# Performance work log

Hardware: AMD Instinct MI355X
Metric: run time of the kernel (lower is better)

## Reference

```python
import jax, jax.numpy as jnp
import numpy as np
from itertools import product

G = 96          # voxel grid side
B = 2           # batch samples
N_PER = 60000   # occupied voxels per sample
N = B * N_PER
C_IN = 64
C_OUT = 1
NUM_BLOCKS = 2
EPS = 1e-5


def _build_kernel_map():
    """Emulate MinkowskiEngine's coordinate hash map for a k=3, stride=1, 3D conv.
    Returns batch_ids [N], and per-offset (in_idx, out_idx) padded to N with sentinel N."""
    rng = np.random.default_rng(0)
    side = G - 2  # coords in [1, G-2] so offset coords never wrap
    keys_list = []
    for b in range(B):
        lin = rng.choice(side ** 3, size=N_PER, replace=False)
        x = lin // (side * side) + 1
        y = (lin // side) % side + 1
        z = lin % side + 1
        keys_list.append(b * G ** 3 + x * G * G + y * G + z)
    keys = np.concatenate(keys_list)
    batch_ids = np.repeat(np.arange(B), N_PER).astype(np.int32)
    order = np.argsort(keys)
    skeys = keys[order]
    in_idx = np.full((27, N), N, np.int32)   # sentinel N -> zero-padded feature row
    out_idx = np.full((27, N), N, np.int32)  # sentinel N -> dropped output row
    for k, (dx, dy, dz) in enumerate(product((-1, 0, 1), repeat=3)):
        nk = keys + dx * G * G + dy * G + dz  # neighbor coordinate key per output voxel
        pos = np.searchsorted(skeys, nk)
        pc = np.clip(pos, 0, N - 1)
        valid = skeys[pc] == nk
        m = int(valid.sum())
        in_idx[k, :m] = order[pc[valid]]
        out_idx[k, :m] = np.nonzero(valid)[0]
    return batch_ids, in_idx, out_idx


def instance_norm(f, batch_ids, num_batches):
    # per-sample, per-channel normalization over all voxels of each sample (ME InstanceNorm, no affine)
    cnt = jax.ops.segment_sum(jnp.ones((f.shape[0],), f.dtype), batch_ids, num_segments=num_batches)
    mean = jax.ops.segment_sum(f, batch_ids, num_segments=num_batches) / cnt[:, None]
    fc = f - mean[batch_ids]
    var = jax.ops.segment_sum(fc * fc, batch_ids, num_segments=num_batches) / cnt[:, None]
    return fc * jax.lax.rsqrt(var + EPS)[batch_ids]


def sparse_conv(f, w, in_idx, out_idx, bias=None):
    # gather-matmul-scatter per kernel offset; w: [27, Cin, Cout]
    n = f.shape[0]
    fpad = jnp.concatenate([f, jnp.zeros((1, f.shape[1]), f.dtype)], axis=0)
    out = jnp.zeros((n + 1, w.shape[-1]), f.dtype)
    for k in range(w.shape[0]):  # static 27-iteration loop over kernel offsets
        out = out.at[out_idx[k]].add(fpad[in_idx[k]] @ w[k])
    out = out[:n]
    if bias is not None:
        out = out + bias
    return out


def setup_inputs() -> dict:
    batch_ids, in_idx, out_idx = _build_kernel_map()
    key = jax.random.key(0)
    k0, k1, k2, k3 = jax.random.split(key, 4)
    feats = jax.random.normal(k0, (N, C_IN), dtype=jnp.float32)
    w_blocks = jax.random.normal(k1, (NUM_BLOCKS, 2, 27, C_IN, C_IN), dtype=jnp.float32) * 0.02
    w_final = jax.random.normal(k2, (27, C_IN, C_OUT), dtype=jnp.float32) * 0.02
    b_final = jax.random.normal(k3, (C_OUT,), dtype=jnp.float32) * 0.02
    return {
        "feats": feats,
        "w_blocks": w_blocks,
        "w_final": w_final,
        "b_final": b_final,
        "in_idx": jnp.asarray(in_idx),
        "out_idx": jnp.asarray(out_idx),
        "batch_ids": jnp.asarray(batch_ids),
        "batch_size": B,
    }


def reference(feats, w_blocks, w_final, b_final, in_idx, out_idx, batch_ids, batch_size):
    # InstanceNorm + ReLU
    x = jax.nn.relu(instance_norm(feats, batch_ids, batch_size))
    # SparseBasicBlocks: conv -> IN -> relu -> conv -> IN -> +res -> relu
    for b in range(w_blocks.shape[0]):
        res = x
        h = sparse_conv(x, w_blocks[b, 0], in_idx, out_idx)
        h = jax.nn.relu(instance_norm(h, batch_ids, batch_size))
        h = sparse_conv(h, w_blocks[b, 1], in_idx, out_idx)
        h = instance_norm(h, batch_ids, batch_size)
        x = jax.nn.relu(h + res)
    # final conv with bias
    return sparse_conv(x, w_final, in_idx, out_idx, bias=b_final)
```

## Files before the change

kernel.cpp:

```cpp
#include <hip/hip_runtime.h>

#define NPTS 120000
#define NROW 120064
#define NB   60000
#define TAPS 27
#define NBLK (NROW / 128)

typedef short  short8 __attribute__((ext_vector_type(8)));
typedef float  f32x4  __attribute__((ext_vector_type(4)));
typedef unsigned int u32;

__device__ __forceinline__ float bf2f(unsigned short u) {
  unsigned v = ((unsigned)u) << 16;
  float f; __builtin_memcpy(&f, &v, 4); return f;
}
__device__ __forceinline__ unsigned short f2bf(float f) {
  unsigned v; __builtin_memcpy(&v, &f, 4);
  v = v + 0x7FFFu + ((v >> 16) & 1u);
  return (unsigned short)(v >> 16);
}

__device__ __forceinline__ int xcd_swz(int orig, int nwg) {
  int q = nwg >> 3, r = nwg & 7;
  int x = orig & 7, i = orig >> 3;
  return (x < r ? x * (q + 1) : r * (q + 1) + (x - r) * q) + i;
}

__global__ __launch_bounds__(256) void k_init(int* __restrict__ nbr,
                                              const float* __restrict__ w,
                                              unsigned short* __restrict__ wp,
                                              float* __restrict__ SMa) {
  int b = blockIdx.x, t = threadIdx.x;
  if (b < 12663) {
    nbr[b * 256 + t] = -1;
    return;
  }
  b -= 12663;
  if (b < 1728) {
    int g = b * 256 + t;
    int e = g & 7, l = (g >> 3) & 63, f = (g >> 9) & 7, rest = g >> 12;
    int tt = f >> 1, h = f & 1;
    int kk = h * 32 + (l >> 4) * 8 + e;
    int cc = tt * 16 + (l & 15);
    wp[g] = f2bf(w[(rest * 64 + kk) * 64 + cc]);
    return;
  }
  if (t < 1280) SMa[t] = 0.f;
}

__global__ __launch_bounds__(256) void k_build_nbr(const int* __restrict__ oi,
                                                   const int* __restrict__ ii,
                                                   int* __restrict__ nbr) {
  int g = blockIdx.x * 256 + threadIdx.x;
  if (g >= TAPS * NPTS) return;
  int o = oi[g];
  if (o < NPTS) nbr[(g / NPTS) * NROW + o] = ii[g];
}

__global__ __launch_bounds__(256) void k_stats1_f32(const float* __restrict__ F,
                                                    float* __restrict__ SM) {
  int lane = threadIdx.x & 63, wave = threadIdx.x >> 6;
  int batch = blockIdx.x >> 7, bb = blockIdx.x & 127;
  const float* Fb = F + (size_t)batch * NB * 64;
  float s = 0.f, ss = 0.f;
  for (int r = bb * 4 + wave; r < NB; r += 512) {
    float v = Fb[(size_t)r * 64 + lane];
    s += v; ss += v * v;
  }
  __shared__ float ls[4][64], lss[4][64];
  ls[wave][lane] = s; lss[wave][lane] = ss;
  __syncthreads();
  if (threadIdx.x < 64) {
    float S  = ls[0][lane] + ls[1][lane] + ls[2][lane] + ls[3][lane];
    float SS = lss[0][lane] + lss[1][lane] + lss[2][lane] + lss[3][lane];
    atomicAdd(&SM[(batch * 2 + 0) * 64 + lane], S);
    atomicAdd(&SM[(batch * 2 + 1) * 64 + lane], SS);
  }
}

__global__ __launch_bounds__(256) void k_apply_f2b(const float* __restrict__ F,
                                                   const float* __restrict__ SM,
                                                   unsigned short* __restrict__ O) {
  int i = blockIdx.x * 256 + threadIdx.x;
  int r = i >> 3, cb = (i & 7) * 8;
  int b = (r >= NB) ? 1 : 0;
  f32x4 v0 = *((const f32x4*)F + i * 2);
  f32x4 v1 = *((const f32x4*)F + i * 2 + 1);
  short8 o;
#pragma unroll
  for (int e = 0; e < 8; ++e) {
    float mean = SM[(b * 2 + 0) * 64 + cb + e] * (1.f / NB);
    float var  = SM[(b * 2 + 1) * 64 + cb + e] * (1.f / NB) - mean * mean;
    float rstd = rsqrtf(var + 1e-5f);
    float x = (e < 4) ? v0[e & 3] : v1[e & 3];
    o[e] = (short)f2bf(fmaxf((x - mean) * rstd, 0.f));
  }
  *((short8*)O + i) = o;
}

__global__ __launch_bounds__(256) void k_apply_bf(const unsigned short* __restrict__ F,
                                                  const float* __restrict__ SM,
                                                  unsigned short* __restrict__ O) {
  int i = blockIdx.x * 256 + threadIdx.x;
  int r = i >> 3, cb = (i & 7) * 8;
  int b = (r >= NB) ? 1 : 0;
  short8 v = *((const short8*)F + i);
  short8 o;
#pragma unroll
  for (int e = 0; e < 8; ++e) {
    float mean = SM[(b * 2 + 0) * 64 + cb + e] * (1.f / NB);
    float var  = SM[(b * 2 + 1) * 64 + cb + e] * (1.f / NB) - mean * mean;
    float rstd = rsqrtf(var + 1e-5f);
    float f = (bf2f((unsigned short)v[e]) - mean) * rstd;
    o[e] = (short)f2bf(fmaxf(f, 0.f));
  }
  *((short8*)O + i) = o;
}

__global__ __launch_bounds__(256) void k_apply_res_bf(const unsigned short* __restrict__ H2,
                                                      const float* __restrict__ SM,
                                                      unsigned short* __restrict__ X) {
  int i = blockIdx.x * 256 + threadIdx.x;
  int r = i >> 3, cb = (i & 7) * 8;
  int b = (r >= NB) ? 1 : 0;
  short8 v = *((const short8*)H2 + i);
  short8 xv = *((const short8*)X + i);
  short8 o;
#pragma unroll
  for (int e = 0; e < 8; ++e) {
    float mean = SM[(b * 2 + 0) * 64 + cb + e] * (1.f / NB);
    float var  = SM[(b * 2 + 1) * 64 + cb + e] * (1.f / NB) - mean * mean;
    float rstd = rsqrtf(var + 1e-5f);
    float f = (bf2f((unsigned short)v[e]) - mean) * rstd + bf2f((unsigned short)xv[e]);
    o[e] = (short)f2bf(fmaxf(f, 0.f));
  }
  *((short8*)X + i) = o;
}

__global__ __launch_bounds__(256) void k_conv64s(const unsigned short* __restrict__ X,
                                                 const unsigned short* __restrict__ WP,
                                                 const int* __restrict__ nbr,
                                                 unsigned short* __restrict__ Y,
                                                 float* __restrict__ SM) {
  const int blk = xcd_swz(blockIdx.x, NBLK);
  const int lane = threadIdx.x & 63, wave = threadIdx.x >> 6;
  const int j0w = blk * 128 + wave * 32;
  const int lrow = lane & 15, lk = lane >> 4;
  f32x4 acc[2][4];
#pragma unroll
  for (int g = 0; g < 2; ++g)
#pragma unroll
    for (int c = 0; c < 4; ++c) acc[g][c] = (f32x4){0.f, 0.f, 0.f, 0.f};

  for (int k = 0; k < TAPS; ++k) {
    const int* np = nbr + (size_t)k * NROW + j0w + lrow;
    int i0 = np[0], i1 = np[16];
    if (__ballot(i0 >= 0 || i1 >= 0) == 0ull) continue;
    short8 a00 = {0,0,0,0,0,0,0,0}, a01 = {0,0,0,0,0,0,0,0};
    short8 a10 = {0,0,0,0,0,0,0,0}, a11 = {0,0,0,0,0,0,0,0};
    if (i0 >= 0) {
      const unsigned short* rp = X + (size_t)i0 * 64 + lk * 8;
      a00 = *(const short8*)rp; a01 = *(const short8*)(rp + 32);
    }
    if (i1 >= 0) {
      const unsigned short* rp = X + (size_t)i1 * 64 + lk * 8;
      a10 = *(const short8*)rp; a11 = *(const short8*)(rp + 32);
    }
    const unsigned short* wpk = WP + k * 4096 + lane * 8;
#pragma unroll
    for (int ct = 0; ct < 4; ++ct) {
      short8 b0 = *(const short8*)(wpk + ct * 1024);
      short8 b1 = *(const short8*)(wpk + ct * 1024 + 512);
      acc[0][ct] = __builtin_amdgcn_mfma_f32_16x16x32_bf16(a00, b0, acc[0][ct], 0, 0, 0);
      acc[0][ct] = __builtin_amdgcn_mfma_f32_16x16x32_bf16(a01, b1, acc[0][ct], 0, 0, 0);
      acc[1][ct] = __builtin_amdgcn_mfma_f32_16x16x32_bf16(a10, b0, acc[1][ct], 0, 0, 0);
      acc[1][ct] = __builtin_amdgcn_mfma_f32_16x16x32_bf16(a11, b1, acc[1][ct], 0, 0, 0);
    }
  }

#pragma unroll
  for (int g = 0; g < 2; ++g) {
    unsigned short* yp = Y + (size_t)(j0w + g * 16 + lk * 4) * 64 + lrow;
#pragma unroll
    for (int r = 0; r < 4; ++r) {
      yp[r * 64 +  0] = f2bf(acc[g][0][r]);
      yp[r * 64 + 16] = f2bf(acc[g][1][r]);
      yp[r * 64 + 32] = f2bf(acc[g][2][r]);
      yp[r * 64 + 48] = f2bf(acc[g][3][r]);
    }
  }

  float s[4][2], q[4][2];
#pragma unroll
  for (int ct = 0; ct < 4; ++ct) { s[ct][0] = s[ct][1] = q[ct][0] = q[ct][1] = 0.f; }
#pragma unroll
  for (int g = 0; g < 2; ++g) {
    int rowbase = j0w + g * 16 + lk * 4;
#pragma unroll
    for (int r = 0; r < 4; ++r) {
      int bt = (rowbase + r) >= NB;
#pragma unroll
      for (int ct = 0; ct < 4; ++ct) {
        float v = acc[g][ct][r];
        s[ct][bt] += v; q[ct][bt] += v * v;
      }
    }
  }
  __shared__ float sred[4][4][4][64];
#pragma unroll
  for (int ct = 0; ct < 4; ++ct)
#pragma unroll
    for (int b = 0; b < 2; ++b) {
      sred[wave][lk][b * 2 + 0][ct * 16 + lrow] = s[ct][b];
      sred[wave][lk][b * 2 + 1][ct * 16 + lrow] = q[ct][b];
    }
  __syncthreads();
  int t = threadIdx.x;
  float S = 0.f;
#pragma unroll
  for (int w = 0; w < 4; ++w)
#pragma unroll
    for (int l2 = 0; l2 < 4; ++l2)
      S += sred[w][l2][t >> 6][t & 63];
  atomicAdd(&SM[t], S);
}

__global__ __launch_bounds__(256) void k_dfin(const unsigned short* __restrict__ X,
                                              const float* __restrict__ WF,
                                              float* __restrict__ D) {
  const int lane = threadIdx.x & 63, wave = threadIdx.x >> 6;
  const int j0 = blockIdx.x * 64 + wave * 16;
  const int lrow = lane & 15, lk = lane >> 4;
  const unsigned short* rp = X + (size_t)(j0 + lrow) * 64 + lk * 8;
  short8 a0 = *(const short8*)rp;
  short8 a1 = *(const short8*)(rp + 32);
  short8 b[2][2];
#pragma unroll
  for (int ct = 0; ct < 2; ++ct) {
    int col = ct * 16 + lrow;
#pragma unroll
    for (int h = 0; h < 2; ++h) {
#pragma unroll
      for (int e = 0; e < 8; ++e)
        b[ct][h][e] = (col < TAPS) ? (short)f2bf(WF[col * 64 + h * 32 + lk * 8 + e]) : (short)0;
    }
  }
  f32x4 acc0 = {0,0,0,0}, acc1 = {0,0,0,0};
  acc0 = __builtin_amdgcn_mfma_f32_16x16x32_bf16(a0, b[0][0], acc0, 0, 0, 0);
  acc0 = __builtin_amdgcn_mfma_f32_16x16x32_bf16(a1, b[0][1], acc0, 0, 0, 0);
  acc1 = __builtin_amdgcn_mfma_f32_16x16x32_bf16(a0, b[1][0], acc1, 0, 0, 0);
  acc1 = __builtin_amdgcn_mfma_f32_16x16x32_bf16(a1, b[1][1], acc1, 0, 0, 0);
  float* dp0 = D + (size_t)lrow * NROW + j0 + lk * 4;
  float* dp1 = D + (size_t)(16 + lrow) * NROW + j0 + lk * 4;
#pragma unroll
  for (int r = 0; r < 4; ++r) { dp0[r] = acc0[r]; dp1[r] = acc1[r]; }
}

__global__ __launch_bounds__(256) void k_gfin(const float* __restrict__ D,
                                              const int* __restrict__ nbr,
                                              const float* __restrict__ BF,
                                              float* __restrict__ out) {
  int j = xcd_swz(blockIdx.x, NROW / 256) * 256 + threadIdx.x;
  if (j >= NPTS) return;
  float acc = BF[0];
#pragma unroll
  for (int k = 0; k < TAPS; ++k) {
    int idx = nbr[(size_t)k * NROW + j];
    if (idx >= 0) acc += D[(size_t)k * NROW + idx];
  }
  out[j] = acc;
}

extern "C" void kernel_launch(void* const* d_in, const int* in_sizes, int n_in,
                              void* d_out, int out_size, void* d_ws, size_t ws_size,
                              hipStream_t stream) {
  (void)in_sizes; (void)n_in; (void)out_size; (void)ws_size;
  const float* feats = (const float*)d_in[0];
  const float* wblk  = (const float*)d_in[1];
  const float* wfin  = (const float*)d_in[2];
  const float* bfin  = (const float*)d_in[3];
  const int* in_idx  = (const int*)d_in[4];
  const int* out_idx = (const int*)d_in[5];

  char* p = (char*)d_ws;
  size_t off = 0;
  auto carve = [&](size_t bytes) {
    void* r = p + off; off += (bytes + 255) & ~(size_t)255; return r;
  };
  int*            nbr = (int*)carve((size_t)TAPS * NROW * 4);
  unsigned short* Xb  = (unsigned short*)carve((size_t)NROW * 64 * 2);
  unsigned short* Hb  = (unsigned short*)carve((size_t)NROW * 64 * 2);
  unsigned short* H2b = (unsigned short*)carve((size_t)NROW * 64 * 2);
  unsigned short* WP  = (unsigned short*)carve(108u * 4096u * 2);
  float*          D   = (float*)carve((size_t)32 * NROW * 4);
  float*          SMa = (float*)carve(5 * 256 * 4);

  float* SM0 = SMa;
  float* SM1 = SMa + 256;
  float* SM2 = SMa + 512;
  float* SM3 = SMa + 768;
  float* SM4 = SMa + 1024;

  k_init<<<12663 + 1728 + 1, 256, 0, stream>>>(nbr, wblk, WP, SMa);
  k_build_nbr<<<(TAPS * NPTS + 255) / 256, 256, 0, stream>>>(out_idx, in_idx, nbr);

  k_stats1_f32<<<256, 256, 0, stream>>>(feats, SM0);
  k_apply_f2b<<<3750, 256, 0, stream>>>(feats, SM0, Xb);

  k_conv64s<<<NBLK, 256, 0, stream>>>(Xb, WP + 0 * 110592, nbr, Hb, SM1);
  k_apply_bf<<<3750, 256, 0, stream>>>(Hb, SM1, Hb);
  k_conv64s<<<NBLK, 256, 0, stream>>>(Hb, WP + 1 * 110592, nbr, H2b, SM2);
  k_apply_res_bf<<<3750, 256, 0, stream>>>(H2b, SM2, Xb);

  k_conv64s<<<NBLK, 256, 0, stream>>>(Xb, WP + 2 * 110592, nbr, Hb, SM3);
  k_apply_bf<<<3750, 256, 0, stream>>>(Hb, SM3, Hb);
  k_conv64s<<<NBLK, 256, 0, stream>>>(Hb, WP + 3 * 110592, nbr, H2b, SM4);
  k_apply_res_bf<<<3750, 256, 0, stream>>>(H2b, SM4, Xb);

  k_dfin<<<NROW / 64, 256, 0, stream>>>(Xb, wfin, D);
  k_gfin<<<NROW / 256, 256, 0, stream>>>(D, nbr, bfin, (float*)d_out);
}
```

Baseline: 474.9 us.

## Fuse instance-norm+ReLU into next conv's gather, prefetch neighbor indices, drop XCD swizzle

Removes the standalone k_apply_bf pass by normalizing and ReLU-ing gathered bf16 rows inside the second conv of each block, using per-channel scale/shift precomputed from the first conv's statistics. The neighbor indices for the next tap are loaded one iteration ahead to hide their latency. The XCD block swizzle is removed from the conv and final-gather kernels. Each gathered row is now normalized up to 27 times instead of once, which adds ALU work in the conv inner loop. Dropping the swizzle may change L2 locality.

```diff
diff --git a/kernel.cpp b/kernel.cpp
--- a/kernel.cpp
+++ b/kernel.cpp
@@ -8,6 +8,7 @@
 
 typedef short  short8 __attribute__((ext_vector_type(8)));
 typedef float  f32x4  __attribute__((ext_vector_type(4)));
+typedef int    int4v  __attribute__((ext_vector_type(4)));
 typedef unsigned int u32;
 
 __device__ __forceinline__ float bf2f(unsigned short u) {
@@ -20,10 +21,19 @@
   return (unsigned short)(v >> 16);
 }
 
-__device__ __forceinline__ int xcd_swz(int orig, int nwg) {
-  int q = nwg >> 3, r = nwg & 7;
-  int x = orig & 7, i = orig >> 3;
-  return (x < r ? x * (q + 1) : r * (q + 1) + (x - r) * q) + i;
+__device__ __forceinline__ short8 norm8(short8 v, const float* A, const float* B) {
+  float f[8];
+#pragma unroll
+  for (int e = 0; e < 8; ++e)
+    f[e] = fmaxf(fmaf(bf2f((unsigned short)v[e]), A[e], B[e]), 0.f);
+  int4v p;
+#pragma unroll
+  for (int j = 0; j < 4; ++j) {
+    u32 r;
+    asm("v_cvt_pk_bf16_f32 %0, %1, %2" : "=v"(r) : "v"(f[2 * j]), "v"(f[2 * j + 1]));
+    p[j] = (int)r;
+  }
+  union { int4v i; short8 s; } u; u.i = p; return u.s;
 }
 
 __global__ __launch_bounds__(256) void k_init(int* __restrict__ nbr,
@@ -98,25 +108,6 @@
   *((short8*)O + i) = o;
 }
 
-__global__ __launch_bounds__(256) void k_apply_bf(const unsigned short* __restrict__ F,
-                                                  const float* __restrict__ SM,
-                                                  unsigned short* __restrict__ O) {
-  int i = blockIdx.x * 256 + threadIdx.x;
-  int r = i >> 3, cb = (i & 7) * 8;
-  int b = (r >= NB) ? 1 : 0;
-  short8 v = *((const short8*)F + i);
-  short8 o;
-#pragma unroll
-  for (int e = 0; e < 8; ++e) {
-    float mean = SM[(b * 2 + 0) * 64 + cb + e] * (1.f / NB);
-    float var  = SM[(b * 2 + 1) * 64 + cb + e] * (1.f / NB) - mean * mean;
-    float rstd = rsqrtf(var + 1e-5f);
-    float f = (bf2f((unsigned short)v[e]) - mean) * rstd;
-    o[e] = (short)f2bf(fmaxf(f, 0.f));
-  }
-  *((short8*)O + i) = o;
-}
-
 __global__ __launch_bounds__(256) void k_apply_res_bf(const unsigned short* __restrict__ H2,
                                                       const float* __restrict__ SM,
                                                       unsigned short* __restrict__ X) {
@@ -137,45 +128,73 @@
   *((short8*)X + i) = o;
 }
 
-__global__ __launch_bounds__(256) void k_conv64s(const unsigned short* __restrict__ X,
+template <int NORM>
+__global__ __launch_bounds__(256) void k_conv64t(const unsigned short* __restrict__ X,
                                                  const unsigned short* __restrict__ WP,
                                                  const int* __restrict__ nbr,
                                                  unsigned short* __restrict__ Y,
+                                                 const float* __restrict__ SMin,
                                                  float* __restrict__ SM) {
-  const int blk = xcd_swz(blockIdx.x, NBLK);
   const int lane = threadIdx.x & 63, wave = threadIdx.x >> 6;
-  const int j0w = blk * 128 + wave * 32;
+  const int j0w = blockIdx.x * 128 + wave * 32;
   const int lrow = lane & 15, lk = lane >> 4;
+
+  float A0[8], B0[8], A1[8], B1[8];
+  if (NORM) {
+    int batch = (j0w >= NB) ? 1 : 0;
+    const float* S0 = SMin + (batch * 2 + 0) * 64;
+    const float* S1 = SMin + (batch * 2 + 1) * 64;
+#pragma unroll
+    for (int e = 0; e < 8; ++e) {
+      int c0 = lk * 8 + e, c1 = 32 + lk * 8 + e;
+      float m0 = S0[c0] * (1.f / NB);
+      float r0 = rsqrtf(S1[c0] * (1.f / NB) - m0 * m0 + 1e-5f);
+      A0[e] = r0; B0[e] = -m0 * r0;
+      float m1 = S0[c1] * (1.f / NB);
+      float r1 = rsqrtf(S1[c1] * (1.f / NB) - m1 * m1 + 1e-5f);
+      A1[e] = r1; B1[e] = -m1 * r1;
+    }
+  }
+
   f32x4 acc[2][4];
 #pragma unroll
   for (int g = 0; g < 2; ++g)
 #pragma unroll
     for (int c = 0; c < 4; ++c) acc[g][c] = (f32x4){0.f, 0.f, 0.f, 0.f};
 
+  const int* np = nbr + j0w + lrow;
+  int i0 = np[0], i1 = np[16];
   for (int k = 0; k < TAPS; ++k) {
-    const int* np = nbr + (size_t)k * NROW + j0w + lrow;
-    int i0 = np[0], i1 = np[16];
-    if (__ballot(i0 >= 0 || i1 >= 0) == 0ull) continue;
-    short8 a00 = {0,0,0,0,0,0,0,0}, a01 = {0,0,0,0,0,0,0,0};
-    short8 a10 = {0,0,0,0,0,0,0,0}, a11 = {0,0,0,0,0,0,0,0};
-    if (i0 >= 0) {
-      const unsigned short* rp = X + (size_t)i0 * 64 + lk * 8;
-      a00 = *(const short8*)rp; a01 = *(const short8*)(rp + 32);
-    }
-    if (i1 >= 0) {
-      const unsigned short* rp = X + (size_t)i1 * 64 + lk * 8;
-      a10 = *(const short8*)rp; a11 = *(const short8*)(rp + 32);
-    }
-    const unsigned short* wpk = WP + k * 4096 + lane * 8;
-#pragma unroll
-    for (int ct = 0; ct < 4; ++ct) {
-      short8 b0 = *(const short8*)(wpk + ct * 1024);
-      short8 b1 = *(const short8*)(wpk + ct * 1024 + 512);
-      acc[0][ct] = __builtin_amdgcn_mfma_f32_16x16x32_bf16(a00, b0, acc[0][ct], 0, 0, 0);
-      acc[0][ct] = __builtin_amdgcn_mfma_f32_16x16x32_bf16(a01, b1, acc[0][ct], 0, 0, 0);
-      acc[1][ct] = __builtin_amdgcn_mfma_f32_16x16x32_bf16(a10, b0, acc[1][ct], 0, 0, 0);
-      acc[1][ct] = __builtin_amdgcn_mfma_f32_16x16x32_bf16(a11, b1, acc[1][ct], 0, 0, 0);
-    }
+    int ni0 = 0, ni1 = 0;
+    if (k + 1 < TAPS) {
+      const int* npn = np + (size_t)(k + 1) * NROW;
+      ni0 = npn[0]; ni1 = npn[16];
+    }
+    if (__ballot(i0 >= 0 || i1 >= 0) != 0ull) {
+      short8 a00 = {0,0,0,0,0,0,0,0}, a01 = {0,0,0,0,0,0,0,0};
+      short8 a10 = {0,0,0,0,0,0,0,0}, a11 = {0,0,0,0,0,0,0,0};
+      if (i0 >= 0) {
+        const unsigned short* rp = X + (size_t)i0 * 64 + lk * 8;
+        a00 = *(const short8*)rp; a01 = *(const short8*)(rp + 32);
+        if (NORM) { a00 = norm8(a00, A0, B0); a01 = norm8(a01, A1, B1); }
+      }
+      if (i1 >= 0) {
+        const unsigned short* rp = X + (size_t)i1 * 64 + lk * 8;
+        a10 = *(const short8*)rp; a11 = *(const short8*)(rp + 32);
+        if (NORM) { a10 = norm8(a10, A0, B0); a11 = norm8(a11, A1, B1); }
+      }
+      const unsigned short* wpk = WP + k * 4096 + lane * 8;
+#pragma unroll
+      for (int ct = 0; ct < 4; ++ct) {
+        short8 b0 = *(const short8*)(wpk + ct * 1024);
+        short8 b1 = *(const short8*)(wpk + ct * 1024 + 512);
+        acc[0][ct] = __builtin_amdgcn_mfma_f32_16x16x32_bf16(a00, b0, acc[0][ct], 0, 0, 0);
+        acc[0][ct] = __builtin_amdgcn_mfma_f32_16x16x32_bf16(a01, b1, acc[0][ct], 0, 0, 0);
+        acc[1][ct] = __builtin_amdgcn_mfma_f32_16x16x32_bf16(a10, b0, acc[1][ct], 0, 0, 0);
+        acc[1][ct] = __builtin_amdgcn_mfma_f32_16x16x32_bf16(a11, b1, acc[1][ct], 0, 0, 0);
+      }
+    }
+    i0 = ni0; i1 = ni1;
   }
 
 #pragma unroll
@@ -260,7 +279,7 @@
                                               const int* __restrict__ nbr,
                                               const float* __restrict__ BF,
                                               float* __restrict__ out) {
-  int j = xcd_swz(blockIdx.x, NROW / 256) * 256 + threadIdx.x;
+  int j = blockIdx.x * 256 + threadIdx.x;
   if (j >= NPTS) return;
   float acc = BF[0];
 #pragma unroll
@@ -307,14 +326,12 @@
   k_stats1_f32<<<256, 256, 0, stream>>>(feats, SM0);
   k_apply_f2b<<<3750, 256, 0, stream>>>(feats, SM0, Xb);
 
-  k_conv64s<<<NBLK, 256, 0, stream>>>(Xb, WP + 0 * 110592, nbr, Hb, SM1);
-  k_apply_bf<<<3750, 256, 0, stream>>>(Hb, SM1, Hb);
-  k_conv64s<<<NBLK, 256, 0, stream>>>(Hb, WP + 1 * 110592, nbr, H2b, SM2);
+  k_conv64t<0><<<NBLK, 256, 0, stream>>>(Xb, WP + 0 * 110592, nbr, Hb, nullptr, SM1);
+  k_conv64t<1><<<NBLK, 256, 0, stream>>>(Hb, WP + 1 * 110592, nbr, H2b, SM1, SM2);
   k_apply_res_bf<<<3750, 256, 0, stream>>>(H2b, SM2, Xb);
 
-  k_conv64s<<<NBLK, 256, 0, stream>>>(Xb, WP + 2 * 110592, nbr, Hb, SM3);
-  k_apply_bf<<<3750, 256, 0, stream>>>(Hb, SM3, Hb);
-  k_conv64s<<<NBLK, 256, 0, stream>>>(Hb, WP + 3 * 110592, nbr, H2b, SM4);
+  k_conv64t<0><<<NBLK, 256, 0, stream>>>(Xb, WP + 2 * 110592, nbr, Hb, nullptr, SM3);
+  k_conv64t<1><<<NBLK, 256, 0, stream>>>(Hb, WP + 3 * 110592, nbr, H2b, SM3, SM4);
   k_apply_res_bf<<<3750, 256, 0, stream>>>(H2b, SM4, Xb);
 
   k_dfin<<<NROW / 64, 256, 0, stream>>>(Xb, wfin, D);
```

Measured after the change: 463.3 us. -2.4%, faster.

## Shrink conv tile to 16 rows per wave and drop XCD block swizzle

Applied to the files above, without the earlier changes.

The sparse conv kernel now gives each wave 16 output rows instead of 32, so each block covers 64 rows and twice as many blocks launch. Per-wave accumulators halve, which lowers register pressure and may raise occupancy. The cost is that each loaded weight fragment now feeds half as many MFMAs, so weight traffic per output doubles. The XCD-aware block swizzle is also removed from the conv and final gather kernels, and the stats-buffer zeroing is fixed to clear all 1280 entries.

```diff
diff --git a/kernel.cpp b/kernel.cpp
--- a/kernel.cpp
+++ b/kernel.cpp
@@ -4,7 +4,7 @@
 #define NROW 120064
 #define NB   60000
 #define TAPS 27
-#define NBLK (NROW / 128)
+#define NBLK (NROW / 64)
 
 typedef short  short8 __attribute__((ext_vector_type(8)));
 typedef float  f32x4  __attribute__((ext_vector_type(4)));
@@ -18,12 +18,6 @@
   unsigned v; __builtin_memcpy(&v, &f, 4);
   v = v + 0x7FFFu + ((v >> 16) & 1u);
   return (unsigned short)(v >> 16);
-}
-
-__device__ __forceinline__ int xcd_swz(int orig, int nwg) {
-  int q = nwg >> 3, r = nwg & 7;
-  int x = orig & 7, i = orig >> 3;
-  return (x < r ? x * (q + 1) : r * (q + 1) + (x - r) * q) + i;
 }
 
 __global__ __launch_bounds__(256) void k_init(int* __restrict__ nbr,
@@ -45,7 +39,8 @@
     wp[g] = f2bf(w[(rest * 64 + kk) * 64 + cc]);
     return;
   }
-  if (t < 1280) SMa[t] = 0.f;
+#pragma unroll
+  for (int j = 0; j < 5; ++j) SMa[j * 256 + t] = 0.f;
 }
 
 __global__ __launch_bounds__(256) void k_build_nbr(const int* __restrict__ oi,
@@ -142,66 +137,51 @@
                                                  const int* __restrict__ nbr,
                                                  unsigned short* __restrict__ Y,
                                                  float* __restrict__ SM) {
-  const int blk = xcd_swz(blockIdx.x, NBLK);
   const int lane = threadIdx.x & 63, wave = threadIdx.x >> 6;
-  const int j0w = blk * 128 + wave * 32;
+  const int j0w = blockIdx.x * 64 + wave * 16;
   const int lrow = lane & 15, lk = lane >> 4;
-  f32x4 acc[2][4];
-#pragma unroll
-  for (int g = 0; g < 2; ++g)
-#pragma unroll
-    for (int c = 0; c < 4; ++c) acc[g][c] = (f32x4){0.f, 0.f, 0.f, 0.f};
+  f32x4 acc[4];
+#pragma unroll
+  for (int c = 0; c < 4; ++c) acc[c] = (f32x4){0.f, 0.f, 0.f, 0.f};
 
   for (int k = 0; k < TAPS; ++k) {
-    const int* np = nbr + (size_t)k * NROW + j0w + lrow;
-    int i0 = np[0], i1 = np[16];
-    if (__ballot(i0 >= 0 || i1 >= 0) == 0ull) continue;
-    short8 a00 = {0,0,0,0,0,0,0,0}, a01 = {0,0,0,0,0,0,0,0};
-    short8 a10 = {0,0,0,0,0,0,0,0}, a11 = {0,0,0,0,0,0,0,0};
-    if (i0 >= 0) {
-      const unsigned short* rp = X + (size_t)i0 * 64 + lk * 8;
-      a00 = *(const short8*)rp; a01 = *(const short8*)(rp + 32);
-    }
-    if (i1 >= 0) {
-      const unsigned short* rp = X + (size_t)i1 * 64 + lk * 8;
-      a10 = *(const short8*)rp; a11 = *(const short8*)(rp + 32);
+    int idx = nbr[(size_t)k * NROW + j0w + lrow];
+    if (__ballot(idx >= 0) == 0ull) continue;
+    short8 a0 = {0,0,0,0,0,0,0,0}, a1 = {0,0,0,0,0,0,0,0};
+    if (idx >= 0) {
+      const unsigned short* rp = X + (size_t)idx * 64 + lk * 8;
+      a0 = *(const short8*)rp; a1 = *(const short8*)(rp + 32);
     }
     const unsigned short* wpk = WP + k * 4096 + lane * 8;
 #pragma unroll
     for (int ct = 0; ct < 4; ++ct) {
       short8 b0 = *(const short8*)(wpk + ct * 1024);
       short8 b1 = *(const short8*)(wpk + ct * 1024 + 512);
-      acc[0][ct] = __builtin_amdgcn_mfma_f32_16x16x32_bf16(a00, b0, acc[0][ct], 0, 0, 0);
-      acc[0][ct] = __builtin_amdgcn_mfma_f32_16x16x32_bf16(a01, b1, acc[0][ct], 0, 0, 0);
-      acc[1][ct] = __builtin_amdgcn_mfma_f32_16x16x32_bf16(a10, b0, acc[1][ct], 0, 0, 0);
-      acc[1][ct] = __builtin_amdgcn_mfma_f32_16x16x32_bf16(a11, b1, acc[1][ct], 0, 0, 0);
-    }
-  }
-
-#pragma unroll
-  for (int g = 0; g < 2; ++g) {
-    unsigned short* yp = Y + (size_t)(j0w + g * 16 + lk * 4) * 64 + lrow;
-#pragma unroll
-    for (int r = 0; r < 4; ++r) {
-      yp[r * 64 +  0] = f2bf(acc[g][0][r]);
-      yp[r * 64 + 16] = f2bf(acc[g][1][r]);
-      yp[r * 64 + 32] = f2bf(acc[g][2][r]);
-      yp[r * 64 + 48] = f2bf(acc[g][3][r]);
-    }
+      acc[ct] = __builtin_amdgcn_mfma_f32_16x16x32_bf16(a0, b0, acc[ct], 0, 0, 0);
+      acc[ct] = __builtin_amdgcn_mfma_f32_16x16x32_bf16(a1, b1, acc[ct], 0, 0, 0);
+    }
+  }
+
+  unsigned short* yp = Y + (size_t)(j0w + lk * 4) * 64 + lrow;
+#pragma unroll
+  for (int r = 0; r < 4; ++r) {
+    yp[r * 64 +  0] = f2bf(acc[0][r]);
+    yp[r * 64 + 16] = f2bf(acc[1][r]);
+    yp[r * 64 + 32] = f2bf(acc[2][r]);
+    yp[r * 64 + 48] = f2bf(acc[3][r]);
   }
 
   float s[4][2], q[4][2];
 #pragma unroll
   for (int ct = 0; ct < 4; ++ct) { s[ct][0] = s[ct][1] = q[ct][0] = q[ct][1] = 0.f; }
-#pragma unroll
-  for (int g = 0; g < 2; ++g) {
-    int rowbase = j0w + g * 16 + lk * 4;
+  {
+    int rowbase = j0w + lk * 4;
 #pragma unroll
     for (int r = 0; r < 4; ++r) {
       int bt = (rowbase + r) >= NB;
 #pragma unroll
       for (int ct = 0; ct < 4; ++ct) {
-        float v = acc[g][ct][r];
+        float v = acc[ct][r];
         s[ct][bt] += v; q[ct][bt] += v * v;
       }
     }
@@ -260,7 +240,7 @@
                                               const int* __restrict__ nbr,
                                               const float* __restrict__ BF,
                                               float* __restrict__ out) {
-  int j = xcd_swz(blockIdx.x, NROW / 256) * 256 + threadIdx.x;
+  int j = blockIdx.x * 256 + threadIdx.x;
   if (j >= NPTS) return;
   float acc = BF[0];
 #pragma unroll
```

Result: slower. 537.1 us (+13.1%).
